# Optimization experiments

Hardware: AMD Instinct MI355X
Metric: run time of the kernel (lower is better)

## Reference

```python
import jax, jax.numpy as jnp
import numpy as np

HEADS = 8
DIM_HEAD = 64
SCALE = DIM_HEAD ** -0.5


def setup_inputs() -> dict:
    key = jax.random.key(0)
    ks = jax.random.split(key, 8)
    B, Nq, Nk, D = 4, 1024, 2048, 512
    inner = HEADS * DIM_HEAD  # 512
    x = jax.random.normal(ks[0], (B, Nq, D), dtype=jnp.float32)
    context = jax.random.normal(ks[1], (B, Nk, D), dtype=jnp.float32)
    bias = jax.random.normal(ks[2], (B, Nq, Nk), dtype=jnp.float32)
    s = D ** -0.5
    Wq = jax.random.normal(ks[3], (inner, D), dtype=jnp.float32) * s
    Wk = jax.random.normal(ks[4], (inner, D), dtype=jnp.float32) * s
    Wv = jax.random.normal(ks[5], (inner, D), dtype=jnp.float32) * s
    Wo = jax.random.normal(ks[6], (D, inner), dtype=jnp.float32) * s
    bo = jnp.zeros((D,), dtype=jnp.float32)
    return {"x": x, "context": context, "bias": bias,
            "Wq": Wq, "Wk": Wk, "Wv": Wv, "Wo": Wo, "bo": bo}


def reference(x, context, bias, Wq, Wk, Wv, Wo, bo):
    B, Nq, _ = x.shape
    # torch Linear: y = x @ W.T ; reshape (h d) -> b h n d
    q = (x @ Wq.T).reshape(B, Nq, HEADS, DIM_HEAD).transpose(0, 2, 1, 3)
    k = (context @ Wk.T).reshape(B, -1, HEADS, DIM_HEAD).transpose(0, 2, 1, 3)
    v = (context @ Wv.T).reshape(B, -1, HEADS, DIM_HEAD).transpose(0, 2, 1, 3)
    # explicit-score fallback path (bias supplied)
    scores = jnp.einsum('bhqd,bhkd->bhqk', q, k) * SCALE
    scores = scores + bias[:, None, :, :]  # 3D bias -> (B,1,Nq,Nk)
    attn = jax.nn.softmax(scores, axis=-1)
    out = jnp.einsum('bhqk,bhkd->bhqd', attn, v)
    out = out.transpose(0, 2, 1, 3).reshape(B, Nq, HEADS * DIM_HEAD)
    return out @ Wo.T + bo
```

## Files before the change

### kernel.cpp

```cpp
#include <hip/hip_runtime.h>

#define H 8
#define DH 64
#define NQ 1024
#define NK 2048
#define DIN 512
#define B 4
#define KSPLIT 2
#define KRANGE (NK / KSPLIT)
#define KTILES (KRANGE / 64)

typedef __bf16 bf16;
typedef __bf16 bf16x8 __attribute__((ext_vector_type(8)));
typedef __bf16 bf16x4 __attribute__((ext_vector_type(4)));
typedef float floatx4 __attribute__((ext_vector_type(4)));

__device__ inline void gload16(const void* g, void* l) {
  __builtin_amdgcn_global_load_lds(
      (const __attribute__((address_space(1))) void*)g,
      (__attribute__((address_space(3))) void*)l, 16, 0, 0);
}

__global__ void cvt_all(const float* __restrict__ x, const float* __restrict__ ctx,
                        const float* __restrict__ wq, const float* __restrict__ wk,
                        const float* __restrict__ wv, const float* __restrict__ wo,
                        bf16* xb, bf16* cb, bf16* wqb, bf16* wkb, bf16* wvb, bf16* wob) {
  long i = ((long)blockIdx.x * 256 + threadIdx.x) * 4;
  const float* s; bf16* d; long o;
  if (i < 2097152)      { s = x;   d = xb;  o = i; }
  else if (i < 6291456) { s = ctx; d = cb;  o = i - 2097152; }
  else if (i < 6553600) { s = wq;  d = wqb; o = i - 6291456; }
  else if (i < 6815744) { s = wk;  d = wkb; o = i - 6553600; }
  else if (i < 7077888) { s = wv;  d = wvb; o = i - 6815744; }
  else                  { s = wo;  d = wob; o = i - 7077888; }
  float4 f = *(const float4*)(s + o);
  bf16x4 v = { (bf16)f.x, (bf16)f.y, (bf16)f.z, (bf16)f.w };
  *(bf16x4*)(d + o) = v;
}

__global__ __launch_bounds__(256) void gemm_qkv(
    const bf16* __restrict__ xb, const bf16* __restrict__ cb,
    const bf16* __restrict__ wqb, const bf16* __restrict__ wkb, const bf16* __restrict__ wvb,
    bf16* __restrict__ qb, bf16* __restrict__ kb, bf16* __restrict__ vtb) {
  const int which = blockIdx.z;
  if (which == 0 && blockIdx.y >= 32) return;
  const bf16* A = (which == 0) ? xb : cb;
  const bf16* W = (which == 0) ? wqb : ((which == 1) ? wkb : wvb);
  bf16* outb = (which == 0) ? qb : ((which == 1) ? kb : vtb);
  const int logT = (which == 0) ? 10 : 11;
  const float scale = (which == 0) ? 0.125f : 1.0f;
  const bool vmode = (which == 2);

  __shared__ bf16 Al[128 * 32];
  __shared__ bf16 Bl[128 * 32];
  const int t = threadIdx.x;
  const int lane = t & 63, w = t >> 6;
  const int ln = lane & 15, quad = lane >> 4;
  const int wm = (w >> 1) * 64, wn = (w & 1) * 64;
  const int rowBase = blockIdx.y * 128;
  const int colBase = blockIdx.x * 128;

  floatx4 acc[4][4] = {};
  const int c0 = t, c1 = t + 256;
  const int r0 = c0 >> 2, o0 = (c0 & 3) * 8;
  const int r1 = c1 >> 2, o1 = (c1 & 3) * 8;
  const bf16* Ab = A + (size_t)rowBase * DIN;
  const bf16* Wb = W + (size_t)colBase * DIN;

  for (int k0 = 0; k0 < DIN; k0 += 32) {
    gload16(Ab + (size_t)r0 * DIN + k0 + o0, &Al[c0 * 8]);
    gload16(Ab + (size_t)r1 * DIN + k0 + o1, &Al[c1 * 8]);
    gload16(Wb + (size_t)r0 * DIN + k0 + o0, &Bl[c0 * 8]);
    gload16(Wb + (size_t)r1 * DIN + k0 + o1, &Bl[c1 * 8]);
    __syncthreads();
    bf16x8 af[4], bfr[4];
#pragma unroll
    for (int i = 0; i < 4; i++)
      af[i] = *(const bf16x8*)&Al[(wm + i * 16 + ln) * 32 + quad * 8];
#pragma unroll
    for (int j = 0; j < 4; j++)
      bfr[j] = *(const bf16x8*)&Bl[(wn + j * 16 + ln) * 32 + quad * 8];
#pragma unroll
    for (int i = 0; i < 4; i++)
#pragma unroll
      for (int j = 0; j < 4; j++)
        acc[i][j] = __builtin_amdgcn_mfma_f32_16x16x32_bf16(af[i], bfr[j], acc[i][j], 0, 0, 0);
    __syncthreads();
  }

  const int T = 1 << logT;
#pragma unroll
  for (int i = 0; i < 4; i++)
#pragma unroll
    for (int j = 0; j < 4; j++)
#pragma unroll
      for (int r = 0; r < 4; r++) {
        const int m = rowBase + wm + i * 16 + quad * 4 + r;
        const int n = colBase + wn + j * 16 + ln;
        const float v = acc[i][j][r] * scale;
        const int bb = m >> logT, tok = m & (T - 1);
        const int hh = n >> 6, d = n & 63;
        if (!vmode)
          outb[((((size_t)(bb * H + hh)) << logT) + tok) * DH + d] = (bf16)v;
        else
          outb[(((size_t)(bb * H + hh) * DH + d) << logT) + tok] = (bf16)v;
      }
}

__global__ __launch_bounds__(256) void gemm_out(
    const bf16* __restrict__ A, const bf16* __restrict__ W,
    float* __restrict__ outf, const float* __restrict__ bo) {
  __shared__ bf16 Al[128 * 32];
  __shared__ bf16 Bl[128 * 32];
  const int t = threadIdx.x;
  const int lane = t & 63, w = t >> 6;
  const int ln = lane & 15, quad = lane >> 4;
  const int wm = (w >> 1) * 64, wn = (w & 1) * 64;
  const int rowBase = blockIdx.y * 128;
  const int colBase = blockIdx.x * 128;

  floatx4 acc[4][4] = {};
  const int c0 = t, c1 = t + 256;
  const int r0 = c0 >> 2, o0 = (c0 & 3) * 8;
  const int r1 = c1 >> 2, o1 = (c1 & 3) * 8;
  const bf16* Ab = A + (size_t)rowBase * DIN;
  const bf16* Wb = W + (size_t)colBase * DIN;

  for (int k0 = 0; k0 < DIN; k0 += 32) {
    gload16(Ab + (size_t)r0 * DIN + k0 + o0, &Al[c0 * 8]);
    gload16(Ab + (size_t)r1 * DIN + k0 + o1, &Al[c1 * 8]);
    gload16(Wb + (size_t)r0 * DIN + k0 + o0, &Bl[c0 * 8]);
    gload16(Wb + (size_t)r1 * DIN + k0 + o1, &Bl[c1 * 8]);
    __syncthreads();
    bf16x8 af[4], bfr[4];
#pragma unroll
    for (int i = 0; i < 4; i++)
      af[i] = *(const bf16x8*)&Al[(wm + i * 16 + ln) * 32 + quad * 8];
#pragma unroll
    for (int j = 0; j < 4; j++)
      bfr[j] = *(const bf16x8*)&Bl[(wn + j * 16 + ln) * 32 + quad * 8];
#pragma unroll
    for (int i = 0; i < 4; i++)
#pragma unroll
      for (int j = 0; j < 4; j++)
        acc[i][j] = __builtin_amdgcn_mfma_f32_16x16x32_bf16(af[i], bfr[j], acc[i][j], 0, 0, 0);
    __syncthreads();
  }

#pragma unroll
  for (int i = 0; i < 4; i++)
#pragma unroll
    for (int j = 0; j < 4; j++)
#pragma unroll
      for (int r = 0; r < 4; r++) {
        const int m = rowBase + wm + i * 16 + quad * 4 + r;
        const int n = colBase + wn + j * 16 + ln;
        outf[(size_t)m * DIN + n] = acc[i][j][r] + bo[n];
      }
}

__global__ __launch_bounds__(256) void attn_fwd(
    const bf16* __restrict__ q, const bf16* __restrict__ k,
    const bf16* __restrict__ vt, const float* __restrict__ bias,
    float* __restrict__ op0, float* __restrict__ op1, float* __restrict__ lpart) {
  __shared__ bf16 KL[64 * 64];
  __shared__ bf16 VL[64 * 64];
  __shared__ float BL[64 * 64];
  __shared__ bf16 Pl[4][16 * 64];
  const int tid = threadIdx.x;
  const int lane = tid & 63, w = tid >> 6;
  const int ln = lane & 15, quad = lane >> 4;
  const int hh = blockIdx.y;
  const int b = blockIdx.z >> 1, ks = blockIdx.z & 1;
  const int q0 = blockIdx.x * 64;
  const int k0 = ks * KRANGE;
  const size_t bh = (size_t)b * H + hh;
  const bf16* qp = q + bh * NQ * DH;
  const bf16* kp = k + bh * NK * DH;
  const bf16* vp = vt + bh * DH * NK;
  const float* bp = bias + ((size_t)b * NQ + q0) * NK;
  bf16* pl = &Pl[w][0];

  bf16x8 qf[2];
#pragma unroll
  for (int kc = 0; kc < 2; kc++)
    qf[kc] = *(const bf16x8*)(qp + (size_t)(q0 + w * 16 + ln) * DH + kc * 32 + quad * 8);

  floatx4 o[4] = {};
  float lacc[4] = {0.f, 0.f, 0.f, 0.f};
  const int lm0 = w * 16 + quad * 4;
  constexpr float L2E = 1.44269504f;
  constexpr float OFF = 34.6246810f;

  for (int tt = 0; tt < KTILES; tt++) {
    const int nk0 = k0 + tt * 64;
#pragma unroll
    for (int s = 0; s < 2; s++) {
      const int i = s * 256 + tid;
      const int r = i >> 3, cc = (i & 7) ^ (r & 7);
      gload16(kp + (size_t)(nk0 + r) * DH + cc * 8, &KL[i * 8]);
      gload16(vp + (size_t)r * NK + nk0 + cc * 8, &VL[i * 8]);
    }
#pragma unroll
    for (int s = 0; s < 4; s++) {
      const int i = s * 256 + tid;
      const int r = i >> 4, cc = (i & 15) ^ (r & 15);
      gload16(bp + (size_t)r * NK + nk0 + cc * 4, &BL[i * 4]);
    }
    __syncthreads();

    floatx4 s4[4] = {};
#pragma unroll
    for (int j = 0; j < 4; j++)
#pragma unroll
      for (int kc = 0; kc < 2; kc++) {
        const int kr = j * 16 + ln;
        bf16x8 kf = *(const bf16x8*)&KL[kr * 64 + (((kc * 4 + quad) ^ (kr & 7)) * 8)];
        s4[j] = __builtin_amdgcn_mfma_f32_16x16x32_bf16(qf[kc], kf, s4[j], 0, 0, 0);
      }

#pragma unroll
    for (int j = 0; j < 4; j++)
#pragma unroll
      for (int r = 0; r < 4; r++) {
        const int lm = lm0 + r;
        const float bv = BL[lm * 64 + (((j * 4 + (ln >> 2)) ^ (lm & 15)) * 4) + (ln & 3)];
        const float p = exp2f(fmaf(s4[j][r] + bv, L2E, -OFF));
        lacc[r] += p;
        s4[j][r] = p;
      }

#pragma unroll
    for (int j = 0; j < 4; j++)
#pragma unroll
      for (int r = 0; r < 4; r++) {
        const int m = quad * 4 + r;
        pl[m * 64 + (((j * 2 + (ln >> 3)) ^ (m & 7)) * 8) + (ln & 7)] = (bf16)s4[j][r];
      }
    asm volatile("s_waitcnt lgkmcnt(0)" ::: "memory");
    bf16x8 pf[2];
#pragma unroll
    for (int kc = 0; kc < 2; kc++)
      pf[kc] = *(const bf16x8*)&pl[ln * 64 + (((kc * 4 + quad) ^ (ln & 7)) * 8)];
#pragma unroll
    for (int jn = 0; jn < 4; jn++)
#pragma unroll
      for (int kc = 0; kc < 2; kc++) {
        const int vr = jn * 16 + ln;
        bf16x8 vf = *(const bf16x8*)&VL[vr * 64 + (((kc * 4 + quad) ^ (vr & 7)) * 8)];
        o[jn] = __builtin_amdgcn_mfma_f32_16x16x32_bf16(pf[kc], vf, o[jn], 0, 0, 0);
      }
    __syncthreads();
  }

#pragma unroll
  for (int d = 1; d < 16; d <<= 1)
#pragma unroll
    for (int r = 0; r < 4; r++)
      lacc[r] += __shfl_xor(lacc[r], d, 64);

  float* op = (ks ? op1 : op0) +
              ((size_t)b * NQ + q0 + w * 16 + quad * 4) * DIN + hh * 64 + ln;
#pragma unroll
  for (int jn = 0; jn < 4; jn++)
#pragma unroll
    for (int r = 0; r < 4; r++)
      op[(size_t)r * DIN + jn * 16] = o[jn][r];

  if (ln == 0) {
    float4 lv = {lacc[0], lacc[1], lacc[2], lacc[3]};
    *(float4*)&lpart[((size_t)ks * B * H + b * H + hh) * NQ + q0 + w * 16 + quad * 4] = lv;
  }
}

__global__ void combine_kernel(const float* __restrict__ op0, const float* __restrict__ op1,
                               const float* __restrict__ lp, bf16* __restrict__ ab) {
  const int i = blockIdx.x * 256 + threadIdx.x;
  const int idx = i * 4;
  const int row = idx >> 9, col = idx & 511;
  const int b = row >> 10, qq = row & 1023, hh = col >> 6;
  const float4 o0 = *(const float4*)(op0 + idx);
  const float4 o1 = *(const float4*)(op1 + idx);
  const float l = lp[(b * H + hh) * NQ + qq] + lp[B * H * NQ + (b * H + hh) * NQ + qq];
  const float inv = 1.0f / l;
  bf16x4 r = { (bf16)((o0.x + o1.x) * inv), (bf16)((o0.y + o1.y) * inv),
               (bf16)((o0.z + o1.z) * inv), (bf16)((o0.w + o1.w) * inv) };
  *(bf16x4*)(ab + idx) = r;
}

extern "C" void kernel_launch(void* const* d_in, const int* in_sizes, int n_in,
                              void* d_out, int out_size, void* d_ws, size_t ws_size,
                              hipStream_t stream) {
  const float* x    = (const float*)d_in[0];
  const float* ctx  = (const float*)d_in[1];
  const float* bias = (const float*)d_in[2];
  const float* Wq   = (const float*)d_in[3];
  const float* Wk   = (const float*)d_in[4];
  const float* Wv   = (const float*)d_in[5];
  const float* Wo   = (const float*)d_in[6];
  const float* bo   = (const float*)d_in[7];
  float* out = (float*)d_out;

  char* p = (char*)d_ws;
  bf16* xb   = (bf16*)(p + 0);
  bf16* cb   = (bf16*)(p + 4194304);
  bf16* wqb  = (bf16*)(p + 12582912);
  bf16* wkb  = (bf16*)(p + 13107200);
  bf16* wvb  = (bf16*)(p + 13631488);
  bf16* wob  = (bf16*)(p + 14155776);
  bf16* qb   = (bf16*)(p + 14680064);
  bf16* kb   = (bf16*)(p + 18874368);
  bf16* vtb  = (bf16*)(p + 27262976);
  bf16* ab   = (bf16*)(p + 35651584);
  float* op1 = (float*)(p + 39845888);
  float* lpart = (float*)(p + 48234496);
  float* op0 = (float*)cb;

  cvt_all<<<7168, 256, 0, stream>>>(x, ctx, Wq, Wk, Wv, Wo, xb, cb, wqb, wkb, wvb, wob);
  gemm_qkv<<<dim3(4, 64, 3), 256, 0, stream>>>(xb, cb, wqb, wkb, wvb, qb, kb, vtb);
  attn_fwd<<<dim3(NQ / 64, H, B * KSPLIT), 256, 0, stream>>>(qb, kb, vtb, bias, op0, op1, lpart);
  combine_kernel<<<2048, 256, 0, stream>>>(op0, op1, lpart, ab);
  gemm_out<<<dim3(4, 32), 256, 0, stream>>>(ab, wob, out, bo);
}
```

Measured before the change: 200.4 us.

## Double-buffer LDS tiles in GEMMs and attention, load bias straight to registers

Both projection GEMMs and the attention kernel now keep two LDS buffers and issue the global-to-LDS loads for the next K tile before computing on the current one, so memory latency can overlap with MFMA work. In attention, the bias tile no longer goes through shared memory. Each lane loads its bias values directly into registers, prefetched one tile ahead, and uses them as the initial MFMA accumulator, which removes the separate bias add. The cost is double the K/V/GEMM LDS footprint and more registers for the bias prefetch, which may reduce occupancy. Bias reads are now less coalesced, with 16-lane 64-byte segments per row.

```diff
diff --git a/kernel.cpp b/kernel.cpp
--- a/kernel.cpp
+++ b/kernel.cpp
@@ -51,8 +51,8 @@
   const float scale = (which == 0) ? 0.125f : 1.0f;
   const bool vmode = (which == 2);
 
-  __shared__ bf16 Al[128 * 32];
-  __shared__ bf16 Bl[128 * 32];
+  __shared__ bf16 Al[2][128 * 32];
+  __shared__ bf16 Bl[2][128 * 32];
   const int t = threadIdx.x;
   const int lane = t & 63, w = t >> 6;
   const int ln = lane & 15, quad = lane >> 4;
@@ -67,19 +67,27 @@
   const bf16* Ab = A + (size_t)rowBase * DIN;
   const bf16* Wb = W + (size_t)colBase * DIN;
 
+  gload16(Ab + (size_t)r0 * DIN + o0, &Al[0][c0 * 8]);
+  gload16(Ab + (size_t)r1 * DIN + o1, &Al[0][c1 * 8]);
+  gload16(Wb + (size_t)r0 * DIN + o0, &Bl[0][c0 * 8]);
+  gload16(Wb + (size_t)r1 * DIN + o1, &Bl[0][c1 * 8]);
+  __syncthreads();
+
   for (int k0 = 0; k0 < DIN; k0 += 32) {
-    gload16(Ab + (size_t)r0 * DIN + k0 + o0, &Al[c0 * 8]);
-    gload16(Ab + (size_t)r1 * DIN + k0 + o1, &Al[c1 * 8]);
-    gload16(Wb + (size_t)r0 * DIN + k0 + o0, &Bl[c0 * 8]);
-    gload16(Wb + (size_t)r1 * DIN + k0 + o1, &Bl[c1 * 8]);
-    __syncthreads();
+    const int cur = (k0 >> 5) & 1, nxt = cur ^ 1;
+    if (k0 + 32 < DIN) {
+      gload16(Ab + (size_t)r0 * DIN + k0 + 32 + o0, &Al[nxt][c0 * 8]);
+      gload16(Ab + (size_t)r1 * DIN + k0 + 32 + o1, &Al[nxt][c1 * 8]);
+      gload16(Wb + (size_t)r0 * DIN + k0 + 32 + o0, &Bl[nxt][c0 * 8]);
+      gload16(Wb + (size_t)r1 * DIN + k0 + 32 + o1, &Bl[nxt][c1 * 8]);
+    }
     bf16x8 af[4], bfr[4];
 #pragma unroll
     for (int i = 0; i < 4; i++)
-      af[i] = *(const bf16x8*)&Al[(wm + i * 16 + ln) * 32 + quad * 8];
-#pragma unroll
-    for (int j = 0; j < 4; j++)
-      bfr[j] = *(const bf16x8*)&Bl[(wn + j * 16 + ln) * 32 + quad * 8];
+      af[i] = *(const bf16x8*)&Al[cur][(wm + i * 16 + ln) * 32 + quad * 8];
+#pragma unroll
+    for (int j = 0; j < 4; j++)
+      bfr[j] = *(const bf16x8*)&Bl[cur][(wn + j * 16 + ln) * 32 + quad * 8];
 #pragma unroll
     for (int i = 0; i < 4; i++)
 #pragma unroll
@@ -110,8 +118,8 @@
 __global__ __launch_bounds__(256) void gemm_out(
     const bf16* __restrict__ A, const bf16* __restrict__ W,
     float* __restrict__ outf, const float* __restrict__ bo) {
-  __shared__ bf16 Al[128 * 32];
-  __shared__ bf16 Bl[128 * 32];
+  __shared__ bf16 Al[2][128 * 32];
+  __shared__ bf16 Bl[2][128 * 32];
   const int t = threadIdx.x;
   const int lane = t & 63, w = t >> 6;
   const int ln = lane & 15, quad = lane >> 4;
@@ -126,19 +134,27 @@
   const bf16* Ab = A + (size_t)rowBase * DIN;
   const bf16* Wb = W + (size_t)colBase * DIN;
 
+  gload16(Ab + (size_t)r0 * DIN + o0, &Al[0][c0 * 8]);
+  gload16(Ab + (size_t)r1 * DIN + o1, &Al[0][c1 * 8]);
+  gload16(Wb + (size_t)r0 * DIN + o0, &Bl[0][c0 * 8]);
+  gload16(Wb + (size_t)r1 * DIN + o1, &Bl[0][c1 * 8]);
+  __syncthreads();
+
   for (int k0 = 0; k0 < DIN; k0 += 32) {
-    gload16(Ab + (size_t)r0 * DIN + k0 + o0, &Al[c0 * 8]);
-    gload16(Ab + (size_t)r1 * DIN + k0 + o1, &Al[c1 * 8]);
-    gload16(Wb + (size_t)r0 * DIN + k0 + o0, &Bl[c0 * 8]);
-    gload16(Wb + (size_t)r1 * DIN + k0 + o1, &Bl[c1 * 8]);
-    __syncthreads();
+    const int cur = (k0 >> 5) & 1, nxt = cur ^ 1;
+    if (k0 + 32 < DIN) {
+      gload16(Ab + (size_t)r0 * DIN + k0 + 32 + o0, &Al[nxt][c0 * 8]);
+      gload16(Ab + (size_t)r1 * DIN + k0 + 32 + o1, &Al[nxt][c1 * 8]);
+      gload16(Wb + (size_t)r0 * DIN + k0 + 32 + o0, &Bl[nxt][c0 * 8]);
+      gload16(Wb + (size_t)r1 * DIN + k0 + 32 + o1, &Bl[nxt][c1 * 8]);
+    }
     bf16x8 af[4], bfr[4];
 #pragma unroll
     for (int i = 0; i < 4; i++)
-      af[i] = *(const bf16x8*)&Al[(wm + i * 16 + ln) * 32 + quad * 8];
-#pragma unroll
-    for (int j = 0; j < 4; j++)
-      bfr[j] = *(const bf16x8*)&Bl[(wn + j * 16 + ln) * 32 + quad * 8];
+      af[i] = *(const bf16x8*)&Al[cur][(wm + i * 16 + ln) * 32 + quad * 8];
+#pragma unroll
+    for (int j = 0; j < 4; j++)
+      bfr[j] = *(const bf16x8*)&Bl[cur][(wn + j * 16 + ln) * 32 + quad * 8];
 #pragma unroll
     for (int i = 0; i < 4; i++)
 #pragma unroll
@@ -163,9 +179,8 @@
     const bf16* __restrict__ q, const bf16* __restrict__ k,
     const bf16* __restrict__ vt, const float* __restrict__ bias,
     float* __restrict__ op0, float* __restrict__ op1, float* __restrict__ lpart) {
-  __shared__ bf16 KL[64 * 64];
-  __shared__ bf16 VL[64 * 64];
-  __shared__ float BL[64 * 64];
+  __shared__ bf16 KL[2][64 * 64];
+  __shared__ bf16 VL[2][64 * 64];
   __shared__ bf16 Pl[4][16 * 64];
   const int tid = threadIdx.x;
   const int lane = tid & 63, w = tid >> 6;
@@ -178,8 +193,12 @@
   const bf16* qp = q + bh * NQ * DH;
   const bf16* kp = k + bh * NK * DH;
   const bf16* vp = vt + bh * DH * NK;
-  const float* bp = bias + ((size_t)b * NQ + q0) * NK;
+  const float* bp = bias + ((size_t)b * NQ + q0 + w * 16 + quad * 4) * NK + ln;
   bf16* pl = &Pl[w][0];
+
+  const int si0 = tid, si1 = tid + 256;
+  const int sr0 = si0 >> 3, sc0 = (si0 & 7) ^ (sr0 & 7);
+  const int sr1 = si1 >> 3, sc1 = (si1 & 7) ^ (sr1 & 7);
 
   bf16x8 qf[2];
 #pragma unroll
@@ -188,34 +207,48 @@
 
   floatx4 o[4] = {};
   float lacc[4] = {0.f, 0.f, 0.f, 0.f};
-  const int lm0 = w * 16 + quad * 4;
+  float bc[4][4], bn[4][4];
   constexpr float L2E = 1.44269504f;
   constexpr float OFF = 34.6246810f;
 
+  gload16(kp + (size_t)(k0 + sr0) * DH + sc0 * 8, &KL[0][si0 * 8]);
+  gload16(kp + (size_t)(k0 + sr1) * DH + sc1 * 8, &KL[0][si1 * 8]);
+  gload16(vp + (size_t)sr0 * NK + k0 + sc0 * 8, &VL[0][si0 * 8]);
+  gload16(vp + (size_t)sr1 * NK + k0 + sc1 * 8, &VL[0][si1 * 8]);
+#pragma unroll
+  for (int j = 0; j < 4; j++)
+#pragma unroll
+    for (int r = 0; r < 4; r++)
+      bc[j][r] = bp[(size_t)r * NK + k0 + j * 16];
+  __syncthreads();
+
   for (int tt = 0; tt < KTILES; tt++) {
-    const int nk0 = k0 + tt * 64;
-#pragma unroll
-    for (int s = 0; s < 2; s++) {
-      const int i = s * 256 + tid;
-      const int r = i >> 3, cc = (i & 7) ^ (r & 7);
-      gload16(kp + (size_t)(nk0 + r) * DH + cc * 8, &KL[i * 8]);
-      gload16(vp + (size_t)r * NK + nk0 + cc * 8, &VL[i * 8]);
+    const int cur = tt & 1, nxt = cur ^ 1;
+    if (tt + 1 < KTILES) {
+      const int nk1 = k0 + (tt + 1) * 64;
+      gload16(kp + (size_t)(nk1 + sr0) * DH + sc0 * 8, &KL[nxt][si0 * 8]);
+      gload16(kp + (size_t)(nk1 + sr1) * DH + sc1 * 8, &KL[nxt][si1 * 8]);
+      gload16(vp + (size_t)sr0 * NK + nk1 + sc0 * 8, &VL[nxt][si0 * 8]);
+      gload16(vp + (size_t)sr1 * NK + nk1 + sc1 * 8, &VL[nxt][si1 * 8]);
+#pragma unroll
+      for (int j = 0; j < 4; j++)
+#pragma unroll
+        for (int r = 0; r < 4; r++)
+          bn[j][r] = bp[(size_t)r * NK + nk1 + j * 16];
     }
-#pragma unroll
-    for (int s = 0; s < 4; s++) {
-      const int i = s * 256 + tid;
-      const int r = i >> 4, cc = (i & 15) ^ (r & 15);
-      gload16(bp + (size_t)r * NK + nk0 + cc * 4, &BL[i * 4]);
+
+    floatx4 s4[4];
+#pragma unroll
+    for (int j = 0; j < 4; j++) {
+      s4[j][0] = bc[j][0]; s4[j][1] = bc[j][1];
+      s4[j][2] = bc[j][2]; s4[j][3] = bc[j][3];
     }
-    __syncthreads();
-
-    floatx4 s4[4] = {};
 #pragma unroll
     for (int j = 0; j < 4; j++)
 #pragma unroll
       for (int kc = 0; kc < 2; kc++) {
         const int kr = j * 16 + ln;
-        bf16x8 kf = *(const bf16x8*)&KL[kr * 64 + (((kc * 4 + quad) ^ (kr & 7)) * 8)];
+        bf16x8 kf = *(const bf16x8*)&KL[cur][kr * 64 + (((kc * 4 + quad) ^ (kr & 7)) * 8)];
         s4[j] = __builtin_amdgcn_mfma_f32_16x16x32_bf16(qf[kc], kf, s4[j], 0, 0, 0);
       }
 
@@ -223,9 +256,7 @@
     for (int j = 0; j < 4; j++)
 #pragma unroll
       for (int r = 0; r < 4; r++) {
-        const int lm = lm0 + r;
-        const float bv = BL[lm * 64 + (((j * 4 + (ln >> 2)) ^ (lm & 15)) * 4) + (ln & 3)];
-        const float p = exp2f(fmaf(s4[j][r] + bv, L2E, -OFF));
+        const float p = exp2f(fmaf(s4[j][r], L2E, -OFF));
         lacc[r] += p;
         s4[j][r] = p;
       }
@@ -247,10 +278,16 @@
 #pragma unroll
       for (int kc = 0; kc < 2; kc++) {
         const int vr = jn * 16 + ln;
-        bf16x8 vf = *(const bf16x8*)&VL[vr * 64 + (((kc * 4 + quad) ^ (vr & 7)) * 8)];
+        bf16x8 vf = *(const bf16x8*)&VL[cur][vr * 64 + (((kc * 4 + quad) ^ (vr & 7)) * 8)];
         o[jn] = __builtin_amdgcn_mfma_f32_16x16x32_bf16(pf[kc], vf, o[jn], 0, 0, 0);
       }
+
     __syncthreads();
+#pragma unroll
+    for (int j = 0; j < 4; j++)
+#pragma unroll
+      for (int r = 0; r < 4; r++)
+        bc[j][r] = bn[j][r];
   }
 
 #pragma unroll
```

Result: no change. 199.7 us (-0.4%).
